# Optimization experiments

Measured on AMD Instinct MI355X. Metric: run time of the kernel, lower is better.

## Reference

```python
import jax, jax.numpy as jnp
import numpy as np

N, C, W_DIM, H_DIM = 2, 256, 64, 64
HEADS = 4
DH = C // HEADS  # per-head dim for Q,K,V projections
EPS = 1e-5


def _layernorm(x, w, b):
    mu = jnp.mean(x, axis=-1, keepdims=True)
    var = jnp.var(x, axis=-1, keepdims=True)
    return (x - mu) * jax.lax.rsqrt(var + EPS) * w + b


def setup_inputs() -> dict:
    key = jax.random.key(0)
    ks = jax.random.split(key, 12)
    s = 1.0 / np.sqrt(C)
    return {
        "x": jax.random.normal(ks[0], (N, C, W_DIM, H_DIM), dtype=jnp.float32),
        "ln1_w": jnp.ones((C,), jnp.float32),
        "ln1_b": jnp.zeros((C,), jnp.float32),
        # per-head projection weights, laid out for x @ W: [heads, C, DH]
        "WQ": jax.random.normal(ks[1], (HEADS, C, DH), jnp.float32) * s,
        "WK": jax.random.normal(ks[2], (HEADS, C, DH), jnp.float32) * s,
        "WV": jax.random.normal(ks[3], (HEADS, C, DH), jnp.float32) * s,
        "ln2_w": jnp.ones((C,), jnp.float32),
        "ln2_b": jnp.zeros((C,), jnp.float32),
        "W1": jax.random.normal(ks[4], (C, C), jnp.float32) * s,
        "b1": jnp.zeros((C,), jnp.float32),
        "W2": jax.random.normal(ks[5], (C, C), jnp.float32) * s,
        "b2": jnp.zeros((C,), jnp.float32),
    }


def reference(x, ln1_w, ln1_b, WQ, WK, WV, ln2_w, ln2_b, W1, b1, W2, b2):
    n, c, w, h = x.shape
    s = w * h
    # 'n c w h -> n (w h) c'
    r = x.reshape(n, c, s).transpose(0, 2, 1)          # [n, s, c]
    norm = _layernorm(r, ln1_w, ln1_b)
    # all heads at once (original loops over heads)
    Q = jnp.einsum('nsc,hcd->nhsd', norm, WQ)
    K = jnp.einsum('nsc,hcd->nhsd', norm, WK)
    V = jnp.einsum('nsc,hcd->nhsd', norm, WV)
    # scale is 1/sqrt(seq_len) per original (keys.shape[1])
    y = jnp.einsum('nhqd,nhkd->nhqk', Q, K) / jnp.sqrt(jnp.float32(s))
    # QUIRK: softmax over dim=1 of [n, q, k] => the QUERY axis (axis=2 here)
    z = jax.nn.softmax(y, axis=2)
    attn = jnp.einsum('nhqk,nhkd->nhqd', z, V)         # [n, h, s, dh]
    attn_cat = attn.transpose(0, 2, 1, 3).reshape(n, s, c)
    out = attn_cat + r
    out = _layernorm(out, ln2_w, ln2_b)
    out = jax.nn.gelu(out @ W1 + b1, approximate=False) @ W2 + b2
    out = out + attn_cat
    # 'n (w h) c -> n c w h'
    return out.transpose(0, 2, 1).reshape(n, c, w, h)
```

## Files before the change

kernel.cpp:

```cpp
#include <hip/hip_runtime.h>
#include <math.h>

#define SEQ 4096
#define CH  256
#define NHT 8
#define DHD 64

#define QSCALE 0.0225421092f

using bf16x8 = __attribute__((ext_vector_type(8))) short;
using f32x4  = __attribute__((ext_vector_type(4))) float;
typedef unsigned short u16;
typedef unsigned int   u32;

__device__ __forceinline__ u16 f2bf(float f) {
    u32 u = __float_as_uint(f);
    u = (u + 0x7fffu + ((u >> 16) & 1u)) >> 16;
    return (u16)u;
}
__device__ __forceinline__ float bf2f(u16 h) {
    return __uint_as_float(((u32)h) << 16);
}

__global__ __launch_bounds__(256) void k_prep(const float* __restrict__ x,
                                              const float* __restrict__ ln1w,
                                              const float* __restrict__ ln1b,
                                              const float* __restrict__ WQ,
                                              const float* __restrict__ WK,
                                              const float* __restrict__ WV,
                                              const float* __restrict__ W1,
                                              const float* __restrict__ W2,
                                              u16* __restrict__ norm,
                                              u16* __restrict__ BtQKV,
                                              u16* __restrict__ W1t,
                                              u16* __restrict__ W2t)
{
    __shared__ float tile[32][257];
    __shared__ float mu[32], rs[32];
    int bid = blockIdx.x;
    int t = threadIdx.x;
    if (bid < 1280) {
        int id = bid * 256 + t;
        if (id < 768 * 256) {
            int j = id >> 8, c = id & 255;
            int which = j >> 8, h = (j >> 6) & 3, d = j & 63;
            const float* W = (which == 0) ? WQ : (which == 1) ? WK : WV;
            BtQKV[id] = f2bf(W[(h * 256 + c) * 64 + d]);
        } else if (id < 768 * 256 + 65536) {
            int jj = id - 768 * 256;
            int j = jj >> 8, c = jj & 255;
            W1t[jj] = f2bf(W1[c * 256 + j]);
        } else if (id < 768 * 256 + 2 * 65536) {
            int jj = id - 768 * 256 - 65536;
            int j = jj >> 8, c = jj & 255;
            W2t[jj] = f2bf(W2[c * 256 + j]);
        }
        return;
    }
    int b2i = bid - 1280;
    int n = b2i >> 7, s0 = (b2i & 127) * 32;
    int sl = t & 31, cg = t >> 5;
    for (int cc = 0; cc < 256; cc += 8) {
        int c = cc + cg;
        tile[sl][c] = x[(n * 256 + c) * SEQ + s0 + sl];
    }
    __syncthreads();
    int wv = t >> 6, l = t & 63;
    for (int rr = 0; rr < 8; rr++) {
        int s = wv * 8 + rr;
        float a0 = tile[s][l], a1 = tile[s][l + 64], a2 = tile[s][l + 128], a3 = tile[s][l + 192];
        float sm = a0 + a1 + a2 + a3;
        float sq = a0 * a0 + a1 * a1 + a2 * a2 + a3 * a3;
        for (int off = 32; off; off >>= 1) { sm += __shfl_xor(sm, off); sq += __shfl_xor(sq, off); }
        if (l == 0) {
            float m = sm * (1.f / 256.f);
            mu[s] = m;
            rs[s] = rsqrtf(sq * (1.f / 256.f) - m * m + 1e-5f);
        }
    }
    __syncthreads();
    float ww = ln1w[t], bb = ln1b[t];
    for (int s = 0; s < 32; s++) {
        float v = (tile[s][t] - mu[s]) * rs[s] * ww + bb;
        norm[(n * SEQ + s0 + s) * 256 + t] = f2bf(v);
    }
}

__global__ __launch_bounds__(256) void k_qkv(const u16* __restrict__ norm,
                                             const u16* __restrict__ Bt,
                                             u16* __restrict__ Qo,
                                             u16* __restrict__ Ko,
                                             u16* __restrict__ Vo)
{
    int m0 = blockIdx.x * 64, j0 = blockIdx.y * 128;
    int t = threadIdx.x, w = t >> 6, lane = t & 63, quad = lane >> 4, l16 = lane & 15;
    const u16* Ap = norm + (long)(m0 + w * 16 + l16) * 256;
    const u16* Bp = Bt + (long)j0 * 256;
    f32x4 z = {0.f, 0.f, 0.f, 0.f};
    f32x4 acc[8];
    #pragma unroll
    for (int j = 0; j < 8; j++) acc[j] = z;
    #pragma unroll
    for (int kc = 0; kc < 8; kc++) {
        bf16x8 a = *(const bf16x8*)&Ap[kc * 32 + quad * 8];
        #pragma unroll
        for (int j = 0; j < 8; j++) {
            bf16x8 b = *(const bf16x8*)&Bp[(long)(j * 16 + l16) * 256 + kc * 32 + quad * 8];
            acc[j] = __builtin_amdgcn_mfma_f32_16x16x32_bf16(a, b, acc[j], 0, 0, 0);
        }
    }
    #pragma unroll
    for (int j = 0; j < 8; j++) {
        int col = j0 + j * 16 + l16;
        int which = col >> 8, h = (col >> 6) & 3, d = col & 63;
        u16* dst = (which == 0) ? Qo : (which == 1) ? Ko : Vo;
        float sc = (which == 0) ? QSCALE : 1.0f;
        #pragma unroll
        for (int r = 0; r < 4; r++) {
            int m = m0 + w * 16 + quad * 4 + r;
            int n = m >> 12, s = m & 4095;
            dst[((n * 4 + h) * SEQ + s) * 64 + d] = f2bf(acc[j][r] * sc);
        }
    }
}

__global__ __launch_bounds__(256) void k_pass1(const u16* __restrict__ Q,
                                               const u16* __restrict__ Km,
                                               float* __restrict__ D4)
{
    __shared__ float Dred[128];
    int nh = blockIdx.y, k0 = blockIdx.x * 128, qc = blockIdx.z;
    const u16* Qh = Q + (long)nh * SEQ * 64;
    const u16* Kh = Km + (long)nh * SEQ * 64;
    int t = threadIdx.x, w = t >> 6, lane = t & 63, quad = lane >> 4, l16 = lane & 15;
    bf16x8 Kf[8][2];
    #pragma unroll
    for (int i = 0; i < 8; i++) {
        Kf[i][0] = *(const bf16x8*)&Kh[(k0 + i * 16 + l16) * 64 + quad * 8];
        Kf[i][1] = *(const bf16x8*)&Kh[(k0 + i * 16 + l16) * 64 + 32 + quad * 8];
    }
    if (t < 128) Dred[t] = 0.f;
    f32x4 z = {0.f, 0.f, 0.f, 0.f};
    float Dacc[8][4] = {};
    const int qw0 = qc * 1024 + w * 256;
    bf16x8 b0 = *(const bf16x8*)&Qh[(qw0 + l16) * 64 + quad * 8];
    bf16x8 b1 = *(const bf16x8*)&Qh[(qw0 + l16) * 64 + 32 + quad * 8];
    for (int step = 0; step < 16; step++) {
        int q = qw0 + step * 16;
        bf16x8 n0, n1;
        if (step < 15) {
            n0 = *(const bf16x8*)&Qh[(q + 16 + l16) * 64 + quad * 8];
            n1 = *(const bf16x8*)&Qh[(q + 16 + l16) * 64 + 32 + quad * 8];
        }
        #pragma unroll
        for (int i = 0; i < 8; i++) {
            f32x4 acc = z;
            acc = __builtin_amdgcn_mfma_f32_16x16x32_bf16(Kf[i][0], b0, acc, 0, 0, 0);
            acc = __builtin_amdgcn_mfma_f32_16x16x32_bf16(Kf[i][1], b1, acc, 0, 0, 0);
            #pragma unroll
            for (int r = 0; r < 4; r++) Dacc[i][r] += exp2f(acc[r]);
        }
        b0 = n0; b1 = n1;
    }
    #pragma unroll
    for (int i = 0; i < 8; i++)
        #pragma unroll
        for (int r = 0; r < 4; r++) {
            float v = Dacc[i][r];
            v += __shfl_xor(v, 1); v += __shfl_xor(v, 2);
            v += __shfl_xor(v, 4); v += __shfl_xor(v, 8);
            Dacc[i][r] = v;
        }
    __syncthreads();
    if (l16 == 0) {
        #pragma unroll
        for (int i = 0; i < 8; i++)
            #pragma unroll
            for (int r = 0; r < 4; r++)
                atomicAdd(&Dred[i * 16 + quad * 4 + r], Dacc[i][r]);
    }
    __syncthreads();
    if (t < 128) D4[((long)(qc * NHT + nh)) * SEQ + k0 + t] = Dred[t];
}

__global__ __launch_bounds__(256) void k_scaleV(const u16* __restrict__ V,
                                                const float* __restrict__ D4,
                                                u16* __restrict__ Vt)
{
    __shared__ float tile[64][65];
    int nh = blockIdx.y, k0 = blockIdx.x * 64;
    int t = threadIdx.x;
    int d = t & 63, kk = t >> 6;
    const u16* Vh = V + (long)nh * SEQ * 64;
    for (int p = 0; p < 16; p++) {
        int k = p * 4 + kk;
        float Dv = D4[((long)(0 * NHT + nh)) * SEQ + k0 + k]
                 + D4[((long)(1 * NHT + nh)) * SEQ + k0 + k]
                 + D4[((long)(2 * NHT + nh)) * SEQ + k0 + k]
                 + D4[((long)(3 * NHT + nh)) * SEQ + k0 + k];
        tile[k][d] = bf2f(Vh[(k0 + k) * 64 + d]) * (1.f / Dv);
    }
    __syncthreads();
    int k2 = t & 63, d4 = t >> 6;
    u16* Vth = Vt + (long)nh * 64 * SEQ;
    for (int p = 0; p < 16; p++) {
        int dd = p * 4 + d4;
        Vth[dd * SEQ + k0 + k2] = f2bf(tile[k2][dd]);
    }
}

__global__ __launch_bounds__(256) void k_pass2(const u16* __restrict__ Q,
                                               const u16* __restrict__ Km,
                                               const u16* __restrict__ Vt,
                                               float* __restrict__ acat2)
{
    __shared__ __align__(16) unsigned char smem[34816];
    u16 (*lP)[64][36] = (u16(*)[64][36])smem;
    float (*SA)[68] = (float(*)[68])smem;
    float (*SB)[68] = (float(*)[68])(smem + 17408);

    int nh = blockIdx.y, q0 = blockIdx.x * 64, kcid = blockIdx.z;
    int n = nh >> 2, h = nh & 3;
    const u16* Qh = Q + (long)nh * SEQ * 64;
    const u16* Kh = Km + (long)nh * SEQ * 64;
    const u16* Vh = Vt + (long)nh * 64 * SEQ;
    int t = threadIdx.x, w = t >> 6, lane = t & 63, quad = lane >> 4, l16 = lane & 15;
    bf16x8 Qf[4][2];
    #pragma unroll
    for (int jq = 0; jq < 4; jq++)
        #pragma unroll
        for (int ch = 0; ch < 2; ch++)
            Qf[jq][ch] = *(const bf16x8*)&Qh[(q0 + jq * 16 + l16) * 64 + ch * 32 + quad * 8];
    f32x4 z = {0.f, 0.f, 0.f, 0.f};
    f32x4 accO[4][4];
    #pragma unroll
    for (int jq = 0; jq < 4; jq++)
        #pragma unroll
        for (int jd = 0; jd < 4; jd++) accO[jq][jd] = z;

    const int kw0 = kcid * 2048 + w * 512;
    bf16x8 kA[2][2], nA[2][2];
    #pragma unroll
    for (int ksub = 0; ksub < 2; ksub++) {
        kA[ksub][0] = *(const bf16x8*)&Kh[(kw0 + ksub * 16 + l16) * 64 + quad * 8];
        kA[ksub][1] = *(const bf16x8*)&Kh[(kw0 + ksub * 16 + l16) * 64 + 32 + quad * 8];
    }
    for (int step = 0; step < 16; step++) {
        int k0 = kw0 + step * 32;
        if (step < 15) {
            #pragma unroll
            for (int ksub = 0; ksub < 2; ksub++) {
                nA[ksub][0] = *(const bf16x8*)&Kh[(k0 + 32 + ksub * 16 + l16) * 64 + quad * 8];
                nA[ksub][1] = *(const bf16x8*)&Kh[(k0 + 32 + ksub * 16 + l16) * 64 + 32 + quad * 8];
            }
        }
        #pragma unroll
        for (int ksub = 0; ksub < 2; ksub++) {
            #pragma unroll
            for (int jq = 0; jq < 4; jq++) {
                f32x4 acc = z;
                acc = __builtin_amdgcn_mfma_f32_16x16x32_bf16(kA[ksub][0], Qf[jq][0], acc, 0, 0, 0);
                acc = __builtin_amdgcn_mfma_f32_16x16x32_bf16(kA[ksub][1], Qf[jq][1], acc, 0, 0, 0);
                u32 e0 = __float_as_uint(exp2f(acc[0]));
                u32 e1 = __float_as_uint(exp2f(acc[1]));
                u32 e2 = __float_as_uint(exp2f(acc[2]));
                u32 e3 = __float_as_uint(exp2f(acc[3]));
                uint2 pk;
                pk.x = __builtin_amdgcn_perm(e1, e0, 0x07060302u);
                pk.y = __builtin_amdgcn_perm(e3, e2, 0x07060302u);
                *(uint2*)&lP[w][jq * 16 + l16][ksub * 16 + quad * 4] = pk;
            }
        }
        #pragma unroll
        for (int jq = 0; jq < 4; jq++) {
            bf16x8 pa = *(const bf16x8*)&lP[w][jq * 16 + l16][quad * 8];
            #pragma unroll
            for (int jd = 0; jd < 4; jd++) {
                bf16x8 vb = *(const bf16x8*)&Vh[(jd * 16 + l16) * SEQ + k0 + quad * 8];
                accO[jq][jd] = __builtin_amdgcn_mfma_f32_16x16x32_bf16(pa, vb, accO[jq][jd], 0, 0, 0);
            }
        }
        #pragma unroll
        for (int ksub = 0; ksub < 2; ksub++) {
            kA[ksub][0] = nA[ksub][0];
            kA[ksub][1] = nA[ksub][1];
        }
    }
    __syncthreads();
    if (w >= 2) {
        float (*S)[68] = (w == 2) ? SA : SB;
        #pragma unroll
        for (int jq = 0; jq < 4; jq++)
            #pragma unroll
            for (int jd = 0; jd < 4; jd++)
                #pragma unroll
                for (int r = 0; r < 4; r++)
                    S[jq * 16 + quad * 4 + r][jd * 16 + l16] = accO[jq][jd][r];
    }
    __syncthreads();
    if (w < 2) {
        float (*S)[68] = (w == 0) ? SA : SB;
        #pragma unroll
        for (int jq = 0; jq < 4; jq++)
            #pragma unroll
            for (int jd = 0; jd < 4; jd++)
                #pragma unroll
                for (int r = 0; r < 4; r++) {
                    float v = accO[jq][jd][r] + S[jq * 16 + quad * 4 + r][jd * 16 + l16];
                    S[jq * 16 + quad * 4 + r][jd * 16 + l16] = v;
                }
    }
    __syncthreads();
    float* dst = acat2 + (long)kcid * 8192 * 256;
    #pragma unroll
    for (int p = 0; p < 4; p++) {
        int row = p * 16 + (t >> 4);
        int ch = (t & 15) * 4;
        float4 va = *(float4*)&SA[row][ch];
        float4 vb = *(float4*)&SB[row][ch];
        float4 o = make_float4(va.x + vb.x, va.y + vb.y, va.z + vb.z, va.w + vb.w);
        *(float4*)&dst[((long)n * SEQ + q0 + row) * 256 + h * 64 + ch] = o;
    }
}

__global__ __launch_bounds__(256) void k_ln2(const float* __restrict__ x,
                                             const float* __restrict__ acat2,
                                             const float* __restrict__ w,
                                             const float* __restrict__ b,
                                             u16* __restrict__ h2,
                                             float* __restrict__ acat)
{
    __shared__ float tile[32][257];
    __shared__ float mu[32], rs[32];
    int n = blockIdx.y, s0 = blockIdx.x * 32;
    int t = threadIdx.x;
    int sl = t & 31, cg = t >> 5;
    for (int cc = 0; cc < 256; cc += 8) {
        int c = cc + cg;
        tile[sl][c] = x[(n * 256 + c) * SEQ + s0 + sl];
    }
    __syncthreads();
    const long STRIDE = (long)8192 * 256;
    for (int s = 0; s < 32; s++) {
        long idx = ((long)n * SEQ + s0 + s) * 256 + t;
        float a = acat2[idx] + acat2[idx + STRIDE];
        acat[idx] = a;
        tile[s][t] += a;
    }
    __syncthreads();
    int wv = t >> 6, l = t & 63;
    for (int rr = 0; rr < 8; rr++) {
        int s = wv * 8 + rr;
        float a0 = tile[s][l], a1 = tile[s][l + 64], a2 = tile[s][l + 128], a3 = tile[s][l + 192];
        float sm = a0 + a1 + a2 + a3;
        float sq = a0 * a0 + a1 * a1 + a2 * a2 + a3 * a3;
        for (int off = 32; off; off >>= 1) { sm += __shfl_xor(sm, off); sq += __shfl_xor(sq, off); }
        if (l == 0) {
            float m = sm * (1.f / 256.f);
            mu[s] = m;
            rs[s] = rsqrtf(sq * (1.f / 256.f) - m * m + 1e-5f);
        }
    }
    __syncthreads();
    float ww = w[t], bb = b[t];
    for (int s = 0; s < 32; s++) {
        float v = (tile[s][t] - mu[s]) * rs[s] * ww + bb;
        h2[((long)n * SEQ + s0 + s) * 256 + t] = f2bf(v);
    }
}

__global__ __launch_bounds__(256) void k_mlp(const u16* __restrict__ h2,
                                             const u16* __restrict__ W1t,
                                             const float* __restrict__ b1v,
                                             const u16* __restrict__ W2t,
                                             const float* __restrict__ b2v,
                                             const float* __restrict__ acat,
                                             float* __restrict__ out)
{
    __shared__ __align__(16) unsigned char smem[36864];
    u16 (*lT)[264] = (u16(*)[264])smem;
    float (*LT)[36] = (float(*)[36])smem;

    int m0 = blockIdx.x * 32;
    int t = threadIdx.x, w = t >> 6, lane = t & 63, quad = lane >> 4, l16 = lane & 15;
    f32x4 z = {0.f, 0.f, 0.f, 0.f};

    f32x4 acc[4][2];
    #pragma unroll
    for (int js = 0; js < 4; js++)
        #pragma unroll
        for (int ms = 0; ms < 2; ms++) acc[js][ms] = z;
    #pragma unroll
    for (int kc = 0; kc < 8; kc++) {
        bf16x8 a[4], b[2];
        #pragma unroll
        for (int js = 0; js < 4; js++)
            a[js] = *(const bf16x8*)&W1t[(long)(w * 64 + js * 16 + l16) * 256 + kc * 32 + quad * 8];
        #pragma unroll
        for (int ms = 0; ms < 2; ms++)
            b[ms] = *(const bf16x8*)&h2[(long)(m0 + ms * 16 + l16) * 256 + kc * 32 + quad * 8];
        #pragma unroll
        for (int js = 0; js < 4; js++)
            #pragma unroll
            for (int ms = 0; ms < 2; ms++)
                acc[js][ms] = __builtin_amdgcn_mfma_f32_16x16x32_bf16(a[js], b[ms], acc[js][ms], 0, 0, 0);
    }
    #pragma unroll
    for (int js = 0; js < 4; js++) {
        #pragma unroll
        for (int ms = 0; ms < 2; ms++) {
            u32 e[4];
            #pragma unroll
            for (int r = 0; r < 4; r++) {
                int j = w * 64 + js * 16 + quad * 4 + r;
                float v = acc[js][ms][r] + b1v[j];
                float g = 0.5f * v * (1.f + erff(v * 0.70710678118f));
                u32 u = __float_as_uint(g);
                e[r] = u + 0x7fffu + ((u >> 16) & 1u);
            }
            uint2 pk;
            pk.x = __builtin_amdgcn_perm(e[1], e[0], 0x07060302u);
            pk.y = __builtin_amdgcn_perm(e[3], e[2], 0x07060302u);
            *(uint2*)&lT[ms * 16 + l16][w * 64 + js * 16 + quad * 4] = pk;
        }
    }
    __syncthreads();
    f32x4 acc2[2][4];
    #pragma unroll
    for (int ms = 0; ms < 2; ms++)
        #pragma unroll
        for (int cs = 0; cs < 4; cs++) acc2[ms][cs] = z;
    #pragma unroll
    for (int kc = 0; kc < 8; kc++) {
        bf16x8 pa[2], wb[4];
        #pragma unroll
        for (int ms = 0; ms < 2; ms++)
            pa[ms] = *(const bf16x8*)&lT[ms * 16 + l16][kc * 32 + quad * 8];
        #pragma unroll
        for (int cs = 0; cs < 4; cs++)
            wb[cs] = *(const bf16x8*)&W2t[(long)(w * 64 + cs * 16 + l16) * 256 + kc * 32 + quad * 8];
        #pragma unroll
        for (int ms = 0; ms < 2; ms++)
            #pragma unroll
            for (int cs = 0; cs < 4; cs++)
                acc2[ms][cs] = __builtin_amdgcn_mfma_f32_16x16x32_bf16(pa[ms], wb[cs], acc2[ms][cs], 0, 0, 0);
    }
    __syncthreads();
    #pragma unroll
    for (int ms = 0; ms < 2; ms++)
        #pragma unroll
        for (int cs = 0; cs < 4; cs++) {
            int c = w * 64 + cs * 16 + l16;
            float bj = b2v[c];
            float4 fv;
            float vv[4];
            #pragma unroll
            for (int r = 0; r < 4; r++) {
                int m = m0 + ms * 16 + quad * 4 + r;
                vv[r] = acc2[ms][cs][r] + bj + acat[(long)m * 256 + c];
            }
            fv = make_float4(vv[0], vv[1], vv[2], vv[3]);
            *(float4*)&LT[c][ms * 16 + quad * 4] = fv;
        }
    __syncthreads();
    int n = m0 >> 12, sbase = m0 & 4095;
    #pragma unroll
    for (int p = 0; p < 8; p++) {
        int row = p * 32 + (t >> 3);
        int ch = (t & 7) * 4;
        float4 v = *(float4*)&LT[row][ch];
        *(float4*)&out[((long)n * 256 + row) * SEQ + sbase + ch] = v;
    }
}

extern "C" void kernel_launch(void* const* d_in, const int* in_sizes, int n_in,
                              void* d_out, int out_size, void* d_ws, size_t ws_size,
                              hipStream_t stream) {
    const float* x    = (const float*)d_in[0];
    const float* ln1w = (const float*)d_in[1];
    const float* ln1b = (const float*)d_in[2];
    const float* WQ   = (const float*)d_in[3];
    const float* WK   = (const float*)d_in[4];
    const float* WV   = (const float*)d_in[5];
    const float* ln2w = (const float*)d_in[6];
    const float* ln2b = (const float*)d_in[7];
    const float* W1   = (const float*)d_in[8];
    const float* b1   = (const float*)d_in[9];
    const float* W2   = (const float*)d_in[10];
    const float* b2   = (const float*)d_in[11];
    float* out = (float*)d_out;

    char* p = (char*)d_ws;
    u16* norm   = (u16*)p;   p += (size_t)8192 * 256 * 2;
    u16* BtQKV  = (u16*)p;   p += (size_t)768 * 256 * 2;
    u16* W1t    = (u16*)p;   p += (size_t)256 * 256 * 2;
    u16* W2t    = (u16*)p;   p += (size_t)256 * 256 * 2;
    u16* Qb     = (u16*)p;   p += (size_t)NHT * SEQ * 64 * 2;
    u16* Kb     = (u16*)p;   p += (size_t)NHT * SEQ * 64 * 2;
    u16* Vb     = (u16*)p;   p += (size_t)NHT * SEQ * 64 * 2;
    float* D4   = (float*)p; p += (size_t)4 * NHT * SEQ * 4;
    u16* Vt     = (u16*)p;   p += (size_t)NHT * SEQ * 64 * 2;
    float* acat2= (float*)p; p += (size_t)2 * 8192 * 256 * 4;
    float* acat = (float*)p; p += (size_t)8192 * 256 * 4;
    u16* h2     = (u16*)p;   p += (size_t)8192 * 256 * 2;

    k_prep<<<1536, 256, 0, stream>>>(x, ln1w, ln1b, WQ, WK, WV, W1, W2,
                                     norm, BtQKV, W1t, W2t);
    k_qkv<<<dim3(128, 6), 256, 0, stream>>>(norm, BtQKV, Qb, Kb, Vb);
    k_pass1<<<dim3(32, 8, 4), 256, 0, stream>>>(Qb, Kb, D4);
    k_scaleV<<<dim3(64, 8), 256, 0, stream>>>(Vb, D4, Vt);
    k_pass2<<<dim3(64, 8, 2), 256, 0, stream>>>(Qb, Kb, Vt, acat2);
    k_ln2<<<dim3(128, 2), 256, 0, stream>>>(x, acat2, ln2w, ln2b, h2, acat);
    k_mlp<<<256, 256, 0, stream>>>(h2, W1t, b1, W2t, b2, acat, out);
}
```

Baseline: 272.5 us.

## Fuse LN2 and MLP into one tail kernel and use hardware exp2

Merges the separate LayerNorm2 and MLP kernels into one k_tail kernel working on 16-row tiles. The normalized activations stay in shared memory, and the residual acat is recomputed from the two acat2 halves, so the acat and h2 intermediates never go through global memory. The kernel also writes the transposed output directly instead of staging it through shared memory. Separately, exp2f in the attention passes is replaced with the raw hardware exp2 builtin to skip denormal and range handling. The costs are smaller M tiles, which reload W1/W2 fragments from global memory more often per row, and slightly different exp2 accuracy at extreme inputs.

```diff
diff --git a/kernel.cpp b/kernel.cpp
--- a/kernel.cpp
+++ b/kernel.cpp
@@ -20,6 +20,9 @@
 }
 __device__ __forceinline__ float bf2f(u16 h) {
     return __uint_as_float(((u32)h) << 16);
+}
+__device__ __forceinline__ float fexp2(float x) {
+    return __builtin_amdgcn_exp2f(x);
 }
 
 __global__ __launch_bounds__(256) void k_prep(const float* __restrict__ x,
@@ -158,7 +161,7 @@
             acc = __builtin_amdgcn_mfma_f32_16x16x32_bf16(Kf[i][0], b0, acc, 0, 0, 0);
             acc = __builtin_amdgcn_mfma_f32_16x16x32_bf16(Kf[i][1], b1, acc, 0, 0, 0);
             #pragma unroll
-            for (int r = 0; r < 4; r++) Dacc[i][r] += exp2f(acc[r]);
+            for (int r = 0; r < 4; r++) Dacc[i][r] += fexp2(acc[r]);
         }
         b0 = n0; b1 = n1;
     }
@@ -261,10 +264,10 @@
                 f32x4 acc = z;
                 acc = __builtin_amdgcn_mfma_f32_16x16x32_bf16(kA[ksub][0], Qf[jq][0], acc, 0, 0, 0);
                 acc = __builtin_amdgcn_mfma_f32_16x16x32_bf16(kA[ksub][1], Qf[jq][1], acc, 0, 0, 0);
-                u32 e0 = __float_as_uint(exp2f(acc[0]));
-                u32 e1 = __float_as_uint(exp2f(acc[1]));
-                u32 e2 = __float_as_uint(exp2f(acc[2]));
-                u32 e3 = __float_as_uint(exp2f(acc[3]));
+                u32 e0 = __float_as_uint(fexp2(acc[0]));
+                u32 e1 = __float_as_uint(fexp2(acc[1]));
+                u32 e2 = __float_as_uint(fexp2(acc[2]));
+                u32 e3 = __float_as_uint(fexp2(acc[3]));
                 uint2 pk;
                 pk.x = __builtin_amdgcn_perm(e1, e0, 0x07060302u);
                 pk.y = __builtin_amdgcn_perm(e3, e2, 0x07060302u);
@@ -323,153 +326,117 @@
     }
 }
 
-__global__ __launch_bounds__(256) void k_ln2(const float* __restrict__ x,
-                                             const float* __restrict__ acat2,
-                                             const float* __restrict__ w,
-                                             const float* __restrict__ b,
-                                             u16* __restrict__ h2,
-                                             float* __restrict__ acat)
-{
-    __shared__ float tile[32][257];
-    __shared__ float mu[32], rs[32];
-    int n = blockIdx.y, s0 = blockIdx.x * 32;
-    int t = threadIdx.x;
-    int sl = t & 31, cg = t >> 5;
-    for (int cc = 0; cc < 256; cc += 8) {
-        int c = cc + cg;
-        tile[sl][c] = x[(n * 256 + c) * SEQ + s0 + sl];
-    }
-    __syncthreads();
+__global__ __launch_bounds__(256) void k_tail(const float* __restrict__ x,
+                                              const float* __restrict__ acat2,
+                                              const float* __restrict__ lnw,
+                                              const float* __restrict__ lnb,
+                                              const u16* __restrict__ W1t,
+                                              const float* __restrict__ b1v,
+                                              const u16* __restrict__ W2t,
+                                              const float* __restrict__ b2v,
+                                              float* __restrict__ out)
+{
+    __shared__ __align__(16) unsigned char smem[16448];
+    float (*tile)[257] = (float(*)[257])smem;
+    u16 (*lT)[264] = (u16(*)[264])smem;
+    __shared__ float mu[16], rs[16];
+    __shared__ __align__(16) u16 lH[16][264];
+
     const long STRIDE = (long)8192 * 256;
-    for (int s = 0; s < 32; s++) {
-        long idx = ((long)n * SEQ + s0 + s) * 256 + t;
-        float a = acat2[idx] + acat2[idx + STRIDE];
-        acat[idx] = a;
-        tile[s][t] += a;
-    }
-    __syncthreads();
-    int wv = t >> 6, l = t & 63;
-    for (int rr = 0; rr < 8; rr++) {
-        int s = wv * 8 + rr;
-        float a0 = tile[s][l], a1 = tile[s][l + 64], a2 = tile[s][l + 128], a3 = tile[s][l + 192];
-        float sm = a0 + a1 + a2 + a3;
-        float sq = a0 * a0 + a1 * a1 + a2 * a2 + a3 * a3;
-        for (int off = 32; off; off >>= 1) { sm += __shfl_xor(sm, off); sq += __shfl_xor(sq, off); }
-        if (l == 0) {
-            float m = sm * (1.f / 256.f);
-            mu[s] = m;
-            rs[s] = rsqrtf(sq * (1.f / 256.f) - m * m + 1e-5f);
-        }
-    }
-    __syncthreads();
-    float ww = w[t], bb = b[t];
-    for (int s = 0; s < 32; s++) {
-        float v = (tile[s][t] - mu[s]) * rs[s] * ww + bb;
-        h2[((long)n * SEQ + s0 + s) * 256 + t] = f2bf(v);
-    }
-}
-
-__global__ __launch_bounds__(256) void k_mlp(const u16* __restrict__ h2,
-                                             const u16* __restrict__ W1t,
-                                             const float* __restrict__ b1v,
-                                             const u16* __restrict__ W2t,
-                                             const float* __restrict__ b2v,
-                                             const float* __restrict__ acat,
-                                             float* __restrict__ out)
-{
-    __shared__ __align__(16) unsigned char smem[36864];
-    u16 (*lT)[264] = (u16(*)[264])smem;
-    float (*LT)[36] = (float(*)[36])smem;
-
-    int m0 = blockIdx.x * 32;
+    int m0 = blockIdx.x * 16;
+    int n = m0 >> 12, s0 = m0 & 4095;
     int t = threadIdx.x, w = t >> 6, lane = t & 63, quad = lane >> 4, l16 = lane & 15;
+
+    {
+        int sl = t & 15, cg = t >> 4;
+        for (int cc = 0; cc < 256; cc += 16) {
+            int c = cc + cg;
+            tile[sl][c] = x[(n * 256 + c) * SEQ + s0 + sl];
+        }
+    }
+    __syncthreads();
+    for (int s = 0; s < 16; s++) {
+        long idx = (long)(m0 + s) * 256 + t;
+        tile[s][t] += acat2[idx] + acat2[idx + STRIDE];
+    }
+    __syncthreads();
+    {
+        int l = t & 63;
+        for (int rr = 0; rr < 4; rr++) {
+            int s = w * 4 + rr;
+            float a0 = tile[s][l], a1 = tile[s][l + 64], a2 = tile[s][l + 128], a3 = tile[s][l + 192];
+            float sm = a0 + a1 + a2 + a3;
+            float sq = a0 * a0 + a1 * a1 + a2 * a2 + a3 * a3;
+            for (int off = 32; off; off >>= 1) { sm += __shfl_xor(sm, off); sq += __shfl_xor(sq, off); }
+            if (l == 0) {
+                float m = sm * (1.f / 256.f);
+                mu[s] = m;
+                rs[s] = rsqrtf(sq * (1.f / 256.f) - m * m + 1e-5f);
+            }
+        }
+    }
+    __syncthreads();
+    {
+        float ww = lnw[t], bb = lnb[t];
+        for (int s = 0; s < 16; s++)
+            lH[s][t] = f2bf((tile[s][t] - mu[s]) * rs[s] * ww + bb);
+    }
+    __syncthreads();
+
     f32x4 z = {0.f, 0.f, 0.f, 0.f};
-
-    f32x4 acc[4][2];
-    #pragma unroll
-    for (int js = 0; js < 4; js++)
-        #pragma unroll
-        for (int ms = 0; ms < 2; ms++) acc[js][ms] = z;
+    f32x4 acc1[4];
+    #pragma unroll
+    for (int js = 0; js < 4; js++) acc1[js] = z;
     #pragma unroll
     for (int kc = 0; kc < 8; kc++) {
-        bf16x8 a[4], b[2];
-        #pragma unroll
-        for (int js = 0; js < 4; js++)
-            a[js] = *(const bf16x8*)&W1t[(long)(w * 64 + js * 16 + l16) * 256 + kc * 32 + quad * 8];
-        #pragma unroll
-        for (int ms = 0; ms < 2; ms++)
-            b[ms] = *(const bf16x8*)&h2[(long)(m0 + ms * 16 + l16) * 256 + kc * 32 + quad * 8];
-        #pragma unroll
-        for (int js = 0; js < 4; js++)
-            #pragma unroll
-            for (int ms = 0; ms < 2; ms++)
-                acc[js][ms] = __builtin_amdgcn_mfma_f32_16x16x32_bf16(a[js], b[ms], acc[js][ms], 0, 0, 0);
+        bf16x8 b = *(const bf16x8*)&lH[l16][kc * 32 + quad * 8];
+        #pragma unroll
+        for (int js = 0; js < 4; js++) {
+            bf16x8 a = *(const bf16x8*)&W1t[(long)(w * 64 + js * 16 + l16) * 256 + kc * 32 + quad * 8];
+            acc1[js] = __builtin_amdgcn_mfma_f32_16x16x32_bf16(a, b, acc1[js], 0, 0, 0);
+        }
     }
     #pragma unroll
     for (int js = 0; js < 4; js++) {
-        #pragma unroll
-        for (int ms = 0; ms < 2; ms++) {
-            u32 e[4];
-            #pragma unroll
-            for (int r = 0; r < 4; r++) {
-                int j = w * 64 + js * 16 + quad * 4 + r;
-                float v = acc[js][ms][r] + b1v[j];
-                float g = 0.5f * v * (1.f + erff(v * 0.70710678118f));
-                u32 u = __float_as_uint(g);
-                e[r] = u + 0x7fffu + ((u >> 16) & 1u);
-            }
-            uint2 pk;
-            pk.x = __builtin_amdgcn_perm(e[1], e[0], 0x07060302u);
-            pk.y = __builtin_amdgcn_perm(e[3], e[2], 0x07060302u);
-            *(uint2*)&lT[ms * 16 + l16][w * 64 + js * 16 + quad * 4] = pk;
-        }
-    }
-    __syncthreads();
-    f32x4 acc2[2][4];
-    #pragma unroll
-    for (int ms = 0; ms < 2; ms++)
-        #pragma unroll
-        for (int cs = 0; cs < 4; cs++) acc2[ms][cs] = z;
+        u32 e[4];
+        #pragma unroll
+        for (int r = 0; r < 4; r++) {
+            int j = w * 64 + js * 16 + quad * 4 + r;
+            float v = acc1[js][r] + b1v[j];
+            float g = 0.5f * v * (1.f + erff(v * 0.70710678118f));
+            u32 u = __float_as_uint(g);
+            e[r] = u + 0x7fffu + ((u >> 16) & 1u);
+        }
+        uint2 pk;
+        pk.x = __builtin_amdgcn_perm(e[1], e[0], 0x07060302u);
+        pk.y = __builtin_amdgcn_perm(e[3], e[2], 0x07060302u);
+        *(uint2*)&lT[l16][w * 64 + js * 16 + quad * 4] = pk;
+    }
+    __syncthreads();
+    f32x4 acc2[4];
+    #pragma unroll
+    for (int cs = 0; cs < 4; cs++) acc2[cs] = z;
     #pragma unroll
     for (int kc = 0; kc < 8; kc++) {
-        bf16x8 pa[2], wb[4];
-        #pragma unroll
-        for (int ms = 0; ms < 2; ms++)
-            pa[ms] = *(const bf16x8*)&lT[ms * 16 + l16][kc * 32 + quad * 8];
-        #pragma unroll
-        for (int cs = 0; cs < 4; cs++)
-            wb[cs] = *(const bf16x8*)&W2t[(long)(w * 64 + cs * 16 + l16) * 256 + kc * 32 + quad * 8];
-        #pragma unroll
-        for (int ms = 0; ms < 2; ms++)
-            #pragma unroll
-            for (int cs = 0; cs < 4; cs++)
-                acc2[ms][cs] = __builtin_amdgcn_mfma_f32_16x16x32_bf16(pa[ms], wb[cs], acc2[ms][cs], 0, 0, 0);
-    }
-    __syncthreads();
-    #pragma unroll
-    for (int ms = 0; ms < 2; ms++)
+        bf16x8 pa = *(const bf16x8*)&lT[l16][kc * 32 + quad * 8];
         #pragma unroll
         for (int cs = 0; cs < 4; cs++) {
-            int c = w * 64 + cs * 16 + l16;
-            float bj = b2v[c];
-            float4 fv;
-            float vv[4];
-            #pragma unroll
-            for (int r = 0; r < 4; r++) {
-                int m = m0 + ms * 16 + quad * 4 + r;
-                vv[r] = acc2[ms][cs][r] + bj + acat[(long)m * 256 + c];
-            }
-            fv = make_float4(vv[0], vv[1], vv[2], vv[3]);
-            *(float4*)&LT[c][ms * 16 + quad * 4] = fv;
-        }
-    __syncthreads();
-    int n = m0 >> 12, sbase = m0 & 4095;
-    #pragma unroll
-    for (int p = 0; p < 8; p++) {
-        int row = p * 32 + (t >> 3);
-        int ch = (t & 7) * 4;
-        float4 v = *(float4*)&LT[row][ch];
-        *(float4*)&out[((long)n * 256 + row) * SEQ + sbase + ch] = v;
+            bf16x8 wb = *(const bf16x8*)&W2t[(long)(w * 64 + cs * 16 + l16) * 256 + kc * 32 + quad * 8];
+            acc2[cs] = __builtin_amdgcn_mfma_f32_16x16x32_bf16(pa, wb, acc2[cs], 0, 0, 0);
+        }
+    }
+    #pragma unroll
+    for (int cs = 0; cs < 4; cs++) {
+        int c = w * 64 + cs * 16 + l16;
+        float bj = b2v[c];
+        float vv[4];
+        #pragma unroll
+        for (int r = 0; r < 4; r++) {
+            long idx = (long)(m0 + quad * 4 + r) * 256 + c;
+            vv[r] = acc2[cs][r] + bj + acat2[idx] + acat2[idx + STRIDE];
+        }
+        float4 o = make_float4(vv[0], vv[1], vv[2], vv[3]);
+        *(float4*)&out[((long)n * 256 + c) * SEQ + s0 + quad * 4] = o;
     }
 }
 
@@ -501,8 +468,6 @@
     float* D4   = (float*)p; p += (size_t)4 * NHT * SEQ * 4;
     u16* Vt     = (u16*)p;   p += (size_t)NHT * SEQ * 64 * 2;
     float* acat2= (float*)p; p += (size_t)2 * 8192 * 256 * 4;
-    float* acat = (float*)p; p += (size_t)8192 * 256 * 4;
-    u16* h2     = (u16*)p;   p += (size_t)8192 * 256 * 2;
 
     k_prep<<<1536, 256, 0, stream>>>(x, ln1w, ln1b, WQ, WK, WV, W1, W2,
                                      norm, BtQKV, W1t, W2t);
@@ -510,6 +475,5 @@
     k_pass1<<<dim3(32, 8, 4), 256, 0, stream>>>(Qb, Kb, D4);
     k_scaleV<<<dim3(64, 8), 256, 0, stream>>>(Vb, D4, Vt);
     k_pass2<<<dim3(64, 8, 2), 256, 0, stream>>>(Qb, Kb, Vt, acat2);
-    k_ln2<<<dim3(128, 2), 256, 0, stream>>>(x, acat2, ln2w, ln2b, h2, acat);
-    k_mlp<<<256, 256, 0, stream>>>(h2, W1t, b1, W2t, b2, acat, out);
-}
+    k_tail<<<512, 256, 0, stream>>>(x, acat2, ln2w, ln2b, W1t, b1, W2t, b2, out);
+}
```

Result: faster. 257.6 us (-5.5%).
